# Optimization experiments

Hardware: AMD Instinct MI355X
Metric: run time of the kernel (lower is better)

Reference implementation:

```python
import jax, jax.numpy as jnp
import numpy as np

EMBED = 1024
HEADS = 16
HEAD_DIM = EMBED // HEADS


def setup_inputs() -> dict:
    key = jax.random.key(0)
    ks = jax.random.split(key, 5)
    x = jax.random.normal(ks[0], (4, 2048, EMBED), dtype=jnp.float32)
    s = 1.0 / np.sqrt(EMBED)
    W_qkv = jax.random.normal(ks[1], (EMBED, 3 * EMBED), dtype=jnp.float32) * s
    b_qkv = jnp.zeros((3 * EMBED,), dtype=jnp.float32)
    W_proj = jax.random.normal(ks[2], (EMBED, EMBED), dtype=jnp.float32) * s
    b_proj = jnp.zeros((EMBED,), dtype=jnp.float32)
    return {"x": x, "W_qkv": W_qkv, "b_qkv": b_qkv, "W_proj": W_proj, "b_proj": b_proj}


def reference(x, W_qkv, b_qkv, W_proj, b_proj):
    B, S, E = x.shape
    scale = 1.0 / np.sqrt(HEAD_DIM)
    qkv = x @ W_qkv + b_qkv                      # [B,S,3E]
    qkv = qkv.reshape(B, S, 3, HEADS, HEAD_DIM)
    q, k, v = qkv[:, :, 0], qkv[:, :, 1], qkv[:, :, 2]   # [B,S,H,D]
    scores = jnp.einsum('bshd,bthd->bhst', q, k) * scale  # [B,H,S,S]
    attn = jax.nn.softmax(scores, axis=-1)
    out = jnp.einsum('bhst,bthd->bshd', attn, v)          # [B,S,H,D]
    out = out.reshape(B, S, E)
    return out @ W_proj + b_proj
```

## Files before the change

kernel.cpp:

```cpp
#include <hip/hip_runtime.h>
#include <math.h>

#define EMBED 1024
#define HEADS 16
#define HD    64
#define SEQ   2048
#define BATCH 4
#define ROWS  (BATCH * SEQ)

typedef _Float16 f16;
typedef __attribute__((ext_vector_type(8))) _Float16 f16x8;
typedef __attribute__((ext_vector_type(4))) _Float16 f16x4;
typedef __attribute__((ext_vector_type(2))) _Float16 f16x2;
typedef __attribute__((ext_vector_type(4))) float    fx4;

typedef __attribute__((address_space(3))) char  lds_char;
typedef __attribute__((address_space(1))) const char glb_char;

#define SCALE_Q 0.18033688011112042f

__global__ __launch_bounds__(256) void prep(const float* __restrict__ x,
                                            f16* __restrict__ x_h,
                                            const float* __restrict__ Wqkv,
                                            f16* __restrict__ Wqt,
                                            const float* __restrict__ Wproj,
                                            f16* __restrict__ Wpt) {
    const int blk = blockIdx.x;
    if (blk < 8192) {
        const int i = (blk * 256 + threadIdx.x) * 4;
        const float4 v = *(const float4*)(x + i);
        f16x4 o = {(f16)v.x, (f16)v.y, (f16)v.z, (f16)v.w};
        *(f16x4*)(x_h + i) = o;
        return;
    }
    __shared__ float t[32][33];
    const float* W;
    f16* Wt;
    int N, bx, by;
    if (blk < 8192 + 3072) {
        const int b2 = blk - 8192;
        W = Wqkv; Wt = Wqt; N = 3072; bx = b2 % 96; by = b2 / 96;
    } else {
        const int b2 = blk - 8192 - 3072;
        W = Wproj; Wt = Wpt; N = 1024; bx = b2 % 32; by = b2 / 32;
    }
    const int tx = threadIdx.x & 31, ty = threadIdx.x >> 5;
    const int k0 = by * 32, n0 = bx * 32;
    #pragma unroll
    for (int i = 0; i < 4; i++)
        t[ty + i * 8][tx] = W[(size_t)(k0 + ty + i * 8) * N + n0 + tx];
    __syncthreads();
    #pragma unroll
    for (int i = 0; i < 4; i++)
        Wt[(size_t)(n0 + ty + i * 8) * 1024 + k0 + tx] = (f16)t[tx][ty + i * 8];
}

template <int MODE>
__global__ __launch_bounds__(256) void gemm_f16k(const f16* __restrict__ A,
                                                 const f16* __restrict__ Bt,
                                                 const float* __restrict__ bias,
                                                 float* __restrict__ Cf,
                                                 f16* __restrict__ qH,
                                                 f16* __restrict__ kH,
                                                 f16* __restrict__ vT,
                                                 int M, int N, int K) {
    __shared__ alignas(16) f16 As[128][32];
    __shared__ alignas(16) f16 Bs[128][32];
    const int tid  = threadIdx.x;
    const int wave = tid >> 6;
    const int lane = tid & 63;
    const int quad = lane >> 4;
    const int l16  = lane & 15;
    const int m0   = blockIdx.y * 128;
    const int n0   = blockIdx.x * 128;
    const int wm   = wave & 1;
    const int wn   = wave >> 1;

    fx4 acc[4][4];
    #pragma unroll
    for (int i = 0; i < 4; i++)
        #pragma unroll
        for (int j = 0; j < 4; j++)
            acc[i][j] = (fx4){0.f, 0.f, 0.f, 0.f};

    lds_char* asb = (lds_char*)&As[0][0];
    lds_char* bsb = (lds_char*)&Bs[0][0];

    for (int k0 = 0; k0 < K; k0 += 32) {
        __syncthreads();
        #pragma unroll
        for (int r = 0; r < 2; r++) {
            const int g   = r * 4 + wave;
            const int c   = g * 64 + lane;
            const int row = c >> 2;
            const int ko  = (c & 3) * 8;
            __builtin_amdgcn_global_load_lds(
                (glb_char*)(A + (size_t)(m0 + row) * K + k0 + ko),
                asb + g * 1024, 16, 0, 0);
            __builtin_amdgcn_global_load_lds(
                (glb_char*)(Bt + (size_t)(n0 + row) * K + k0 + ko),
                bsb + g * 1024, 16, 0, 0);
        }
        __syncthreads();

        f16x8 af[4], bf[4];
        #pragma unroll
        for (int t = 0; t < 4; t++) {
            af[t] = *(const f16x8*)&As[wm * 64 + t * 16 + l16][quad * 8];
            bf[t] = *(const f16x8*)&Bs[wn * 64 + t * 16 + l16][quad * 8];
        }
        #pragma unroll
        for (int i = 0; i < 4; i++)
            #pragma unroll
            for (int j = 0; j < 4; j++)
                acc[i][j] = __builtin_amdgcn_mfma_f32_16x16x32_f16(af[i], bf[j], acc[i][j], 0, 0, 0);
    }

    const int region = n0 >> 10;
    #pragma unroll
    for (int i = 0; i < 4; i++) {
        const int mb = m0 + wm * 64 + i * 16 + quad * 4;
        #pragma unroll
        for (int j = 0; j < 4; j++) {
            const int n  = n0 + wn * 64 + j * 16 + l16;
            const float bn = bias[n];
            #pragma unroll
            for (int r = 0; r < 4; r++) {
                const int m = mb + r;
                const float v = acc[i][j][r] + bn;
                if (MODE == 0) {
                    Cf[(size_t)m * N + n] = v;
                } else {
                    const int b = m >> 11, s = m & 2047;
                    if (region == 0) {
                        qH[(size_t)m * EMBED + n] = (f16)(v * SCALE_Q);
                    } else if (region == 1) {
                        const int np = n - 1024, hh = np >> 6, d = np & 63;
                        kH[(((size_t)(b * 16 + hh) * SEQ + s) << 6) + d] = (f16)v;
                    } else {
                        const int np = n - 2048, hh = np >> 6, d = np & 63;
                        const int sp = (s & ~31) | ((s & 15) << 1) | ((s >> 4) & 1);
                        vT[((size_t)(b * 16 + hh) * HD + d) * SEQ + sp] = (f16)v;
                    }
                }
            }
        }
    }
}

__global__ __launch_bounds__(256, 4) void attn_mfma(const f16* __restrict__ qH,
                                                    const f16* __restrict__ kH,
                                                    const f16* __restrict__ vT,
                                                    f16* __restrict__ ctx) {
    __shared__ alignas(16) f16 Ks[64 * 64];
    __shared__ alignas(16) f16 Vt[64 * 64];
    __shared__ alignas(16) f16 Pl[4][2][16 * 64];

    const int tid  = threadIdx.x;
    const int wave = tid >> 6;
    const int lane = tid & 63;
    const int quad = lane >> 4;
    const int l16  = lane & 15;

    const int bid = (int)blockIdx.x;
    const int swz = (bid & 7) * 128 + (bid >> 3);
    const int qb = swz & 15;
    const int bh = swz >> 4;
    const int h  = bh & 15;
    const int b  = bh >> 4;
    const int q0 = qb * 128 + wave * 32;

    const f16* kB = kH + (size_t)bh * SEQ * HD;
    const f16* vB = vT + (size_t)bh * HD * SEQ;

    f16x8 qf[2][2];
    #pragma unroll
    for (int s = 0; s < 2; s++) {
        const f16* qp = qH + (size_t)(b * SEQ + q0 + s * 16 + l16) * EMBED + h * HD;
        #pragma unroll
        for (int c = 0; c < 2; c++)
            qf[s][c] = *(const f16x8*)(qp + c * 32 + quad * 8);
    }

    fx4 o[2][4];
    fx4 ls[2];
    #pragma unroll
    for (int s = 0; s < 2; s++) {
        ls[s] = (fx4){0.f, 0.f, 0.f, 0.f};
        #pragma unroll
        for (int dc = 0; dc < 4; dc++)
            o[s][dc] = (fx4){0.f, 0.f, 0.f, 0.f};
    }

    f16x8 ones8;
    #pragma unroll
    for (int j = 0; j < 8; j++) ones8[j] = (f16)1.0f;

    lds_char* ksb = (lds_char*)&Ks[0];
    lds_char* vsb = (lds_char*)&Vt[0];

    auto STAGE_K = [&](int kb) {
        #pragma unroll
        for (int it = 0; it < 2; it++) {
            const int g  = wave * 2 + it;
            const int c  = g * 64 + lane;
            const int r  = c >> 3;
            const int jl = (c & 7) ^ (r & 7);
            __builtin_amdgcn_global_load_lds(
                (glb_char*)(kB + (size_t)(kb * 64 + r) * HD + jl * 8),
                ksb + g * 1024, 16, 0, 0);
        }
    };
    auto STAGE_V = [&](int kb) {
        #pragma unroll
        for (int it = 0; it < 2; it++) {
            const int g  = wave * 2 + it;
            const int c  = g * 64 + lane;
            const int r  = c >> 3;
            const int jl = (c & 7) ^ (r & 7);
            __builtin_amdgcn_global_load_lds(
                (glb_char*)(vB + (size_t)r * SEQ + kb * 64 + jl * 8),
                vsb + g * 1024, 16, 0, 0);
        }
    };

    STAGE_K(0);
    STAGE_V(0);
    __syncthreads();

    for (int kb = 0; kb < SEQ / 64; kb++) {
        fx4 st0[4], st1[4];
        __builtin_amdgcn_s_setprio(1);
        #pragma unroll
        for (int t = 0; t < 4; t++) {
            const int row = l16 + 16 * t;
            const f16x8 kt0 = *(const f16x8*)&Ks[(row * 8 + ((0 + quad) ^ (row & 7))) * 8];
            const f16x8 kt1 = *(const f16x8*)&Ks[(row * 8 + ((4 + quad) ^ (row & 7))) * 8];
            fx4 z = {0.f, 0.f, 0.f, 0.f};
            st0[t] = __builtin_amdgcn_mfma_f32_16x16x32_f16(qf[0][0], kt0, z, 0, 0, 0);
            st0[t] = __builtin_amdgcn_mfma_f32_16x16x32_f16(qf[0][1], kt1, st0[t], 0, 0, 0);
            st1[t] = __builtin_amdgcn_mfma_f32_16x16x32_f16(qf[1][0], kt0, z, 0, 0, 0);
            st1[t] = __builtin_amdgcn_mfma_f32_16x16x32_f16(qf[1][1], kt1, st1[t], 0, 0, 0);
        }
        __builtin_amdgcn_s_setprio(0);

        #pragma unroll
        for (int g = 0; g < 2; g++)
            #pragma unroll
            for (int r = 0; r < 4; r++) {
                const int row = quad * 4 + r;
                const int cc  = (g * 4 + (l16 >> 2)) ^ (row & 7);
                {
                    const float pa = __builtin_amdgcn_exp2f(st0[2 * g][r]);
                    const float pb = __builtin_amdgcn_exp2f(st0[2 * g + 1][r]);
                    const f16x2 pk = __builtin_bit_cast(f16x2, __builtin_amdgcn_cvt_pkrtz(pa, pb));
                    *(f16x2*)&Pl[wave][0][row * 64 + cc * 8 + (l16 & 3) * 2] = pk;
                }
                {
                    const float pa = __builtin_amdgcn_exp2f(st1[2 * g][r]);
                    const float pb = __builtin_amdgcn_exp2f(st1[2 * g + 1][r]);
                    const f16x2 pk = __builtin_bit_cast(f16x2, __builtin_amdgcn_cvt_pkrtz(pa, pb));
                    *(f16x2*)&Pl[wave][1][row * 64 + cc * 8 + (l16 & 3) * 2] = pk;
                }
            }

        __syncthreads();
        if (kb + 1 < SEQ / 64) STAGE_K(kb + 1);

        const f16x8 pf00 = *(const f16x8*)&Pl[wave][0][l16 * 64 + ((0 + quad) ^ (l16 & 7)) * 8];
        const f16x8 pf01 = *(const f16x8*)&Pl[wave][0][l16 * 64 + ((4 + quad) ^ (l16 & 7)) * 8];
        const f16x8 pf10 = *(const f16x8*)&Pl[wave][1][l16 * 64 + ((0 + quad) ^ (l16 & 7)) * 8];
        const f16x8 pf11 = *(const f16x8*)&Pl[wave][1][l16 * 64 + ((4 + quad) ^ (l16 & 7)) * 8];
        __builtin_amdgcn_s_setprio(1);
        #pragma unroll
        for (int dc = 0; dc < 4; dc++) {
            const int row = 16 * dc + l16;
            const f16x8 vf0 = *(const f16x8*)&Vt[(row * 8 + ((0 + quad) ^ (row & 7))) * 8];
            const f16x8 vf1 = *(const f16x8*)&Vt[(row * 8 + ((4 + quad) ^ (row & 7))) * 8];
            o[0][dc] = __builtin_amdgcn_mfma_f32_16x16x32_f16(pf00, vf0, o[0][dc], 0, 0, 0);
            o[0][dc] = __builtin_amdgcn_mfma_f32_16x16x32_f16(pf01, vf1, o[0][dc], 0, 0, 0);
            o[1][dc] = __builtin_amdgcn_mfma_f32_16x16x32_f16(pf10, vf0, o[1][dc], 0, 0, 0);
            o[1][dc] = __builtin_amdgcn_mfma_f32_16x16x32_f16(pf11, vf1, o[1][dc], 0, 0, 0);
        }
        ls[0] = __builtin_amdgcn_mfma_f32_16x16x32_f16(pf00, ones8, ls[0], 0, 0, 0);
        ls[0] = __builtin_amdgcn_mfma_f32_16x16x32_f16(pf01, ones8, ls[0], 0, 0, 0);
        ls[1] = __builtin_amdgcn_mfma_f32_16x16x32_f16(pf10, ones8, ls[1], 0, 0, 0);
        ls[1] = __builtin_amdgcn_mfma_f32_16x16x32_f16(pf11, ones8, ls[1], 0, 0, 0);
        __builtin_amdgcn_s_setprio(0);

        __syncthreads();
        if (kb + 1 < SEQ / 64) STAGE_V(kb + 1);
    }

    #pragma unroll
    for (int s = 0; s < 2; s++) {
        #pragma unroll
        for (int r = 0; r < 4; r++) {
            const float inv = 1.0f / ls[s][r];
            const int q = q0 + s * 16 + quad * 4 + r;
            f16* dst = ctx + (size_t)(b * SEQ + q) * EMBED + h * HD;
            #pragma unroll
            for (int dc = 0; dc < 4; dc++)
                dst[dc * 16 + l16] = (f16)(o[s][dc][r] * inv);
        }
    }
}

extern "C" void kernel_launch(void* const* d_in, const int* in_sizes, int n_in,
                              void* d_out, int out_size, void* d_ws, size_t ws_size,
                              hipStream_t stream) {
    const float* x     = (const float*)d_in[0];
    const float* Wqkv  = (const float*)d_in[1];
    const float* bqkv  = (const float*)d_in[2];
    const float* Wproj = (const float*)d_in[3];
    const float* bproj = (const float*)d_in[4];
    float* out = (float*)d_out;

    f16* x_h = (f16*)d_ws;
    f16* qHb = x_h + (size_t)ROWS * EMBED;
    f16* kHb = qHb + (size_t)ROWS * EMBED;
    f16* vTb = kHb + (size_t)ROWS * EMBED;
    f16* ctx = vTb + (size_t)ROWS * EMBED;
    f16* Wqt = ctx + (size_t)ROWS * EMBED;
    f16* Wpt = Wqt + (size_t)3 * EMBED * EMBED;

    prep<<<dim3(12288), dim3(256), 0, stream>>>(x, x_h, Wqkv, Wqt, Wproj, Wpt);

    gemm_f16k<1><<<dim3(3 * EMBED / 128, ROWS / 128), dim3(256), 0, stream>>>(
        x_h, Wqt, bqkv, nullptr, qHb, kHb, vTb, ROWS, 3 * EMBED, EMBED);

    attn_mfma<<<dim3(64 * 16), dim3(256), 0, stream>>>(qHb, kHb, vTb, ctx);

    gemm_f16k<0><<<dim3(EMBED / 128, ROWS / 128), dim3(256), 0, stream>>>(
        ctx, Wpt, bproj, out, nullptr, nullptr, nullptr, ROWS, EMBED, EMBED);
}
```

Measured before the change: 305.9 us.

## Deepen GEMM K-tile, XOR-swizzle LDS, overlap next stage load with MFMAs

The GEMM K step grows from 32 to 64 per LDS tile, and LDS columns are XOR-swizzled so fragment reads avoid bank conflicts. All fragments are loaded into registers up front, so the next tile's global-to-LDS load can be issued while the second half of the MFMAs runs, hiding load latency. A workgroup index remap groups blocks for better L2 reuse. The cost is more LDS and registers per block.

After: 295.8 us. -3.3%, faster.

```diff
diff --git a/kernel.cpp b/kernel.cpp
--- a/kernel.cpp
+++ b/kernel.cpp
@@ -64,15 +64,21 @@
                                                  f16* __restrict__ kH,
                                                  f16* __restrict__ vT,
                                                  int M, int N, int K) {
-    __shared__ alignas(16) f16 As[128][32];
-    __shared__ alignas(16) f16 Bs[128][32];
+    __shared__ alignas(16) f16 As[128][64];
+    __shared__ alignas(16) f16 Bs[128][64];
     const int tid  = threadIdx.x;
     const int wave = tid >> 6;
     const int lane = tid & 63;
     const int quad = lane >> 4;
     const int l16  = lane & 15;
-    const int m0   = blockIdx.y * 128;
-    const int n0   = blockIdx.x * 128;
+
+    const int nwg  = gridDim.x * gridDim.y;
+    const int flat = blockIdx.y * gridDim.x + blockIdx.x;
+    const int swz  = (flat & 7) * (nwg >> 3) + (flat >> 3);
+    const int bx   = swz % gridDim.x;
+    const int by   = swz / gridDim.x;
+    const int m0   = by * 128;
+    const int n0   = bx * 128;
     const int wm   = wave & 1;
     const int wn   = wave >> 1;
 
@@ -86,34 +92,54 @@
     lds_char* asb = (lds_char*)&As[0][0];
     lds_char* bsb = (lds_char*)&Bs[0][0];
 
-    for (int k0 = 0; k0 < K; k0 += 32) {
-        __syncthreads();
-        #pragma unroll
-        for (int r = 0; r < 2; r++) {
-            const int g   = r * 4 + wave;
-            const int c   = g * 64 + lane;
-            const int row = c >> 2;
-            const int ko  = (c & 3) * 8;
+    const int srow = lane >> 3;
+    const int sjl  = ((lane & 7) ^ (srow & 7)) * 8;
+    auto STAGE = [&](int k0) {
+        #pragma unroll
+        for (int it = 0; it < 4; it++) {
+            const int g = it * 4 + wave;
+            const int r = g * 8 + srow;
             __builtin_amdgcn_global_load_lds(
-                (glb_char*)(A + (size_t)(m0 + row) * K + k0 + ko),
+                (glb_char*)(A + (size_t)(m0 + r) * K + k0 + sjl),
                 asb + g * 1024, 16, 0, 0);
             __builtin_amdgcn_global_load_lds(
-                (glb_char*)(Bt + (size_t)(n0 + row) * K + k0 + ko),
+                (glb_char*)(Bt + (size_t)(n0 + r) * K + k0 + sjl),
                 bsb + g * 1024, 16, 0, 0);
         }
+    };
+
+    STAGE(0);
+    __syncthreads();
+
+    const int NKB = K >> 6;
+    for (int kb = 0; kb < NKB; kb++) {
+        f16x8 af0[4], af1[4], bf0[4], bf1[4];
+        #pragma unroll
+        for (int t = 0; t < 4; t++) {
+            const int ra = wm * 64 + t * 16 + l16;
+            const int rb = wn * 64 + t * 16 + l16;
+            af0[t] = *(const f16x8*)&As[ra][((0 + quad) ^ (ra & 7)) * 8];
+            af1[t] = *(const f16x8*)&As[ra][((4 + quad) ^ (ra & 7)) * 8];
+            bf0[t] = *(const f16x8*)&Bs[rb][((0 + quad) ^ (rb & 7)) * 8];
+            bf1[t] = *(const f16x8*)&Bs[rb][((4 + quad) ^ (rb & 7)) * 8];
+        }
+
+        #pragma unroll
+        for (int i = 0; i < 4; i++)
+            #pragma unroll
+            for (int j = 0; j < 4; j++)
+                acc[i][j] = __builtin_amdgcn_mfma_f32_16x16x32_f16(af0[i], bf0[j], acc[i][j], 0, 0, 0);
+
         __syncthreads();
-
-        f16x8 af[4], bf[4];
-        #pragma unroll
-        for (int t = 0; t < 4; t++) {
-            af[t] = *(const f16x8*)&As[wm * 64 + t * 16 + l16][quad * 8];
-            bf[t] = *(const f16x8*)&Bs[wn * 64 + t * 16 + l16][quad * 8];
-        }
+        if (kb + 1 < NKB) STAGE((kb + 1) << 6);
+
         #pragma unroll
         for (int i = 0; i < 4; i++)
             #pragma unroll
             for (int j = 0; j < 4; j++)
-                acc[i][j] = __builtin_amdgcn_mfma_f32_16x16x32_f16(af[i], bf[j], acc[i][j], 0, 0, 0);
+                acc[i][j] = __builtin_amdgcn_mfma_f32_16x16x32_f16(af1[i], bf1[j], acc[i][j], 0, 0, 0);
+
+        __syncthreads();
     }
 
     const int region = n0 >> 10;
```

## Double-buffer GEMM LDS, swizzle block order, stage V-transpose stores, shrink proj tile

Applied to the files above, without the earlier changes.

The GEMM kernel now double-buffers its LDS tiles so global-to-LDS loads for the next K step are issued while MFMAs run on the current one, and it raises wave priority around the MFMA block. Workgroup indices are remapped so that blocks sharing operand tiles run close together in time, which should improve L2 reuse. The V-transposed output is written through an XOR-swizzled LDS staging buffer to produce coalesced 16-byte stores instead of scattered 2-byte writes. The output-projection GEMM uses a 64-row tile, doubling its block count to fill more CUs, at the cost of less operand reuse per block and more LDS per block.

Result: faster. 282.7 us (-7.6%).

```diff
diff --git a/kernel.cpp b/kernel.cpp
--- a/kernel.cpp
+++ b/kernel.cpp
@@ -64,62 +64,143 @@
                                                  f16* __restrict__ kH,
                                                  f16* __restrict__ vT,
                                                  int M, int N, int K) {
-    __shared__ alignas(16) f16 As[128][32];
-    __shared__ alignas(16) f16 Bs[128][32];
+    constexpr int MI  = (MODE == 0) ? 2 : 4;
+    constexpr int BM  = MI * 32;
+    constexpr int AEL = BM * 32;
+    constexpr int BEL = 128 * 32;
+    __shared__ alignas(16) f16 smem[2 * (AEL + BEL)];
+
+    f16 (*As0)[32] = (f16(*)[32])(smem);
+    f16 (*As1)[32] = (f16(*)[32])(smem + AEL);
+    f16 (*Bs0)[32] = (f16(*)[32])(smem + 2 * AEL);
+    f16 (*Bs1)[32] = (f16(*)[32])(smem + 2 * AEL + BEL);
+    lds_char* a0b = (lds_char*)smem;
+    lds_char* a1b = (lds_char*)smem + AEL * 2;
+    lds_char* b0b = (lds_char*)smem + 4 * AEL;
+    lds_char* b1b = (lds_char*)smem + 4 * AEL + BEL * 2;
+
     const int tid  = threadIdx.x;
     const int wave = tid >> 6;
     const int lane = tid & 63;
     const int quad = lane >> 4;
     const int l16  = lane & 15;
-    const int m0   = blockIdx.y * 128;
-    const int n0   = blockIdx.x * 128;
+
+    const int nwg  = gridDim.x * gridDim.y;
+    const int flat = blockIdx.y * gridDim.x + blockIdx.x;
+    const int swz  = (flat & 7) * (nwg >> 3) + (flat >> 3);
+    const int bx   = swz % gridDim.x;
+    const int by   = swz / gridDim.x;
+    const int m0   = by * BM;
+    const int n0   = bx * 128;
     const int wm   = wave & 1;
     const int wn   = wave >> 1;
 
-    fx4 acc[4][4];
-    #pragma unroll
-    for (int i = 0; i < 4; i++)
+    fx4 acc[MI][4];
+    #pragma unroll
+    for (int i = 0; i < MI; i++)
         #pragma unroll
         for (int j = 0; j < 4; j++)
             acc[i][j] = (fx4){0.f, 0.f, 0.f, 0.f};
 
-    lds_char* asb = (lds_char*)&As[0][0];
-    lds_char* bsb = (lds_char*)&Bs[0][0];
-
-    for (int k0 = 0; k0 < K; k0 += 32) {
-        __syncthreads();
-        #pragma unroll
-        for (int r = 0; r < 2; r++) {
-            const int g   = r * 4 + wave;
-            const int c   = g * 64 + lane;
-            const int row = c >> 2;
-            const int ko  = (c & 3) * 8;
+    const int grow = lane >> 2;
+    const int gcol = (lane & 3) * 8;
+    auto STAGE = [&](lds_char* asb, lds_char* bsb, int k0) {
+        if (MODE == 1) {
+            #pragma unroll
+            for (int r = 0; r < 2; r++) {
+                const int g = r * 4 + wave;
+                __builtin_amdgcn_global_load_lds(
+                    (glb_char*)(A + (size_t)(m0 + g * 16 + grow) * K + k0 + gcol),
+                    asb + g * 1024, 16, 0, 0);
+                __builtin_amdgcn_global_load_lds(
+                    (glb_char*)(Bt + (size_t)(n0 + g * 16 + grow) * K + k0 + gcol),
+                    bsb + g * 1024, 16, 0, 0);
+            }
+        } else {
+            const int ga = wave;
             __builtin_amdgcn_global_load_lds(
-                (glb_char*)(A + (size_t)(m0 + row) * K + k0 + ko),
-                asb + g * 1024, 16, 0, 0);
-            __builtin_amdgcn_global_load_lds(
-                (glb_char*)(Bt + (size_t)(n0 + row) * K + k0 + ko),
-                bsb + g * 1024, 16, 0, 0);
-        }
-        __syncthreads();
-
-        f16x8 af[4], bf[4];
-        #pragma unroll
-        for (int t = 0; t < 4; t++) {
-            af[t] = *(const f16x8*)&As[wm * 64 + t * 16 + l16][quad * 8];
-            bf[t] = *(const f16x8*)&Bs[wn * 64 + t * 16 + l16][quad * 8];
-        }
-        #pragma unroll
-        for (int i = 0; i < 4; i++)
+                (glb_char*)(A + (size_t)(m0 + ga * 16 + grow) * K + k0 + gcol),
+                asb + ga * 1024, 16, 0, 0);
+            #pragma unroll
+            for (int r = 0; r < 2; r++) {
+                const int g = r * 4 + wave;
+                __builtin_amdgcn_global_load_lds(
+                    (glb_char*)(Bt + (size_t)(n0 + g * 16 + grow) * K + k0 + gcol),
+                    bsb + g * 1024, 16, 0, 0);
+            }
+        }
+    };
+
+    auto COMPUTE = [&](f16 (*As)[32], f16 (*Bs)[32]) {
+        f16x8 af[MI], bf[4];
+        #pragma unroll
+        for (int i = 0; i < MI; i++)
+            af[i] = *(const f16x8*)&As[wm * (MI * 16) + i * 16 + l16][quad * 8];
+        #pragma unroll
+        for (int j = 0; j < 4; j++)
+            bf[j] = *(const f16x8*)&Bs[wn * 64 + j * 16 + l16][quad * 8];
+        __builtin_amdgcn_s_setprio(1);
+        #pragma unroll
+        for (int i = 0; i < MI; i++)
             #pragma unroll
             for (int j = 0; j < 4; j++)
                 acc[i][j] = __builtin_amdgcn_mfma_f32_16x16x32_f16(af[i], bf[j], acc[i][j], 0, 0, 0);
-    }
-
-    const int region = n0 >> 10;
-    #pragma unroll
-    for (int i = 0; i < 4; i++) {
-        const int mb = m0 + wm * 64 + i * 16 + quad * 4;
+        __builtin_amdgcn_s_setprio(0);
+    };
+
+    STAGE(a0b, b0b, 0);
+    __syncthreads();
+    STAGE(a1b, b1b, 32);
+
+    const int NT = K >> 5;
+    for (int t = 0; t < NT; t += 2) {
+        COMPUTE(As0, Bs0);
+        __syncthreads();
+        if (t + 2 < NT) STAGE(a0b, b0b, (t + 2) * 32);
+        COMPUTE(As1, Bs1);
+        __syncthreads();
+        if (t + 3 < NT) STAGE(a1b, b1b, (t + 3) * 32);
+    }
+
+    const int region = (MODE == 1) ? (n0 >> 10) : 0;
+
+    if (MODE == 1 && region == 2) {
+        const int b  = m0 >> 11;
+        const int s0 = m0 & 2047;
+        #pragma unroll
+        for (int i = 0; i < MI; i++) {
+            #pragma unroll
+            for (int j = 0; j < 4; j++) {
+                const int nloc = wn * 64 + j * 16 + l16;
+                const float bn = bias[n0 + nloc];
+                #pragma unroll
+                for (int r = 0; r < 4; r++) {
+                    const int sloc = wm * 64 + i * 16 + quad * 4 + r;
+                    const int sp   = (sloc & ~31) | ((sloc & 15) << 1) | ((sloc >> 4) & 1);
+                    const int phys = (sp >> 3) ^ (nloc & 15);
+                    smem[nloc * 128 + phys * 8 + (sp & 7)] = (f16)(acc[i][j][r] + bn);
+                }
+            }
+        }
+        __syncthreads();
+        const int nl = tid >> 1;
+        const int hf = tid & 1;
+        const int np0 = n0 - 2048;
+        f16* dst = vT + ((size_t)(b * 16 + ((np0 + nl) >> 6)) * HD + (nl & 63)) * SEQ
+                      + s0 + hf * 64;
+        #pragma unroll
+        for (int ch = 0; ch < 8; ch++) {
+            const int lc   = hf * 8 + ch;
+            const int phys = lc ^ (nl & 15);
+            const f16x8 v  = *(const f16x8*)&smem[nl * 128 + phys * 8];
+            *(f16x8*)(dst + ch * 8) = v;
+        }
+        return;
+    }
+
+    #pragma unroll
+    for (int i = 0; i < MI; i++) {
+        const int mb = m0 + wm * (MI * 16) + i * 16 + quad * 4;
         #pragma unroll
         for (int j = 0; j < 4; j++) {
             const int n  = n0 + wn * 64 + j * 16 + l16;
@@ -134,13 +215,9 @@
                     const int b = m >> 11, s = m & 2047;
                     if (region == 0) {
                         qH[(size_t)m * EMBED + n] = (f16)(v * SCALE_Q);
-                    } else if (region == 1) {
+                    } else {
                         const int np = n - 1024, hh = np >> 6, d = np & 63;
                         kH[(((size_t)(b * 16 + hh) * SEQ + s) << 6) + d] = (f16)v;
-                    } else {
-                        const int np = n - 2048, hh = np >> 6, d = np & 63;
-                        const int sp = (s & ~31) | ((s & 15) << 1) | ((s >> 4) & 1);
-                        vT[((size_t)(b * 16 + hh) * HD + d) * SEQ + sp] = (f16)v;
                     }
                 }
             }
@@ -331,6 +408,6 @@
 
     attn_mfma<<<dim3(64 * 16), dim3(256), 0, stream>>>(qHb, kHb, vTb, ctx);
 
-    gemm_f16k<0><<<dim3(EMBED / 128, ROWS / 128), dim3(256), 0, stream>>>(
+    gemm_f16k<0><<<dim3(EMBED / 128, ROWS / 64), dim3(256), 0, stream>>>(
         ctx, Wpt, bproj, out, nullptr, nullptr, nullptr, ROWS, EMBED, EMBED);
 }
```
